# Optimization experiments

Measured on AMD Instinct MI355X. Metric: run time of the kernel, lower is better.

Reference implementation:

```python
import jax, jax.numpy as jnp
import numpy as np

HID, H, HKV, D, INT, S, T = 2048, 16, 8, 128, 6144, 4096, 512
POS = 0          # absolute position of the first token in this prefill chunk
EPS = 1e-6
SCALE = 1.0 / D ** 0.5
REP = H // HKV


def setup_inputs() -> dict:
    key = jax.random.key(0)
    ks = jax.random.split(key, 12)
    w = lambda k, sh: jax.random.normal(k, sh, dtype=jnp.float32) * 0.02

    hidden_conv = jax.random.normal(ks[0], (1, HID, 1, T), dtype=jnp.float32)

    # RoPE tables for absolute positions POS..POS+T-1, HF half-rotation layout
    inv_freq = 1.0 / (10000.0 ** (jnp.arange(0, D, 2, dtype=jnp.float32) / D))
    pos = (POS + jnp.arange(T, dtype=jnp.float32))
    ang = pos[:, None] * inv_freq[None, :]                      # (T, D/2)
    emb = jnp.concatenate([ang, ang], axis=-1)                  # (T, D)
    cos = jnp.cos(emb)[None]                                    # (1, T, D)
    sin = jnp.sin(emb)[None]

    # one-hot write mask: column t has a 1 at row POS+t
    update_mask = jnp.zeros((S, T), jnp.float32).at[POS + jnp.arange(T), jnp.arange(T)].set(1.0)[None, None]
    # causal mask over the cache: slot s visible to token t iff s <= POS+t
    attn_mask = jnp.where(jnp.arange(S)[None, :] <= (POS + jnp.arange(T))[:, None], 0.0, -1e4).astype(jnp.float32)[None, None]

    k_cache = jnp.zeros((1, HKV, S, D), jnp.float32)
    v_cache = jnp.zeros((1, HKV, S, D), jnp.float32)

    return dict(
        hidden_conv=hidden_conv, cos=cos, sin=sin,
        update_mask=update_mask, attn_mask=attn_mask,
        k_cache=k_cache, v_cache=v_cache,
        wq=w(ks[1], (H * D, HID)), wk=w(ks[2], (HKV * D, HID)),
        wv=w(ks[3], (HKV * D, HID)), wo=w(ks[4], (HID, H * D)),
        ln1_w=jnp.ones((HID,), jnp.float32), ln2_w=jnp.ones((HID,), jnp.float32),
        qn_w=jnp.ones((D,), jnp.float32), kn_w=jnp.ones((D,), jnp.float32),
        w_gate_up=w(ks[5], (2 * INT, HID)), w_down=w(ks[6], (HID, INT)),
    )


def _rms(x, w):
    return x * jax.lax.rsqrt(jnp.mean(x * x, axis=-1, keepdims=True) + EPS) * w


def _rotate_half(x):
    x1, x2 = jnp.split(x, 2, axis=-1)
    return jnp.concatenate([-x2, x1], axis=-1)


def reference(hidden_conv, cos, sin, update_mask, attn_mask, k_cache, v_cache,
              wq, wk, wv, wo, ln1_w, ln2_w, qn_w, kn_w, w_gate_up, w_down):
    # (1, HID, 1, T) conv layout -> (1, T, HID)
    x = jnp.transpose(hidden_conv[:, :, 0, :], (0, 2, 1))

    h = _rms(x, ln1_w)
    # 1x1 conv == linear; channel order h*D+d matches view(1,H,D,T)
    q = jnp.einsum('btc,oc->bto', h, wq).reshape(1, T, H, D).transpose(0, 2, 1, 3)    # (1,H,T,D)
    k = jnp.einsum('btc,oc->bto', h, wk).reshape(1, T, HKV, D).transpose(0, 2, 1, 3)  # (1,HKV,T,D)
    v = jnp.einsum('btc,oc->bto', h, wv).reshape(1, T, HKV, D).transpose(0, 2, 1, 3)

    q = _rms(q, qn_w)
    k = _rms(k, kn_w)

    cos_b = cos[:, None]  # (1,1,T,D)
    sin_b = sin[:, None]
    q = q * cos_b + _rotate_half(q) * sin_b
    k = k * cos_b + _rotate_half(k) * sin_b

    # matmul-based KV cache write via one-hot mask (faithful to original)
    k_inc = jnp.matmul(update_mask, k)                 # (1,HKV,S,D)
    v_inc = jnp.matmul(update_mask, v)
    write_any = jnp.sum(update_mask, axis=-1, keepdims=True)  # (1,1,S,1)
    k_full = k_cache * (1.0 - write_any) + k_inc
    v_full = v_cache * (1.0 - write_any) + v_inc

    k_rep = jnp.repeat(k_full, REP, axis=1)            # (1,H,S,D)
    v_rep = jnp.repeat(v_full, REP, axis=1)

    scores = jnp.einsum('bhtd,bhsd->bhts', q, k_rep) * SCALE + attn_mask  # (1,H,T,S)
    attn = jax.nn.softmax(scores, axis=-1)
    out = jnp.einsum('bhts,bhsd->bhtd', attn, v_rep)   # (1,H,T,D)

    o_in = out.transpose(0, 2, 1, 3).reshape(1, T, H * D)
    attn_out = jnp.einsum('btc,oc->bto', o_in, wo)
    hidden = x + attn_out

    h2 = _rms(hidden, ln2_w)
    gate_up = jnp.einsum('btc,oc->bto', h2, w_gate_up)
    gate, up = jnp.split(gate_up, 2, axis=-1)
    mlp = jnp.einsum('bti,oi->bto', jax.nn.silu(gate) * up, w_down)
    hidden = hidden + mlp

    hidden_out = jnp.transpose(hidden, (0, 2, 1))[:, :, None, :]  # back to (1,HID,1,T)
    return hidden_out, k_full, v_full


if __name__ == '__main__':
    outs = reference(**setup_inputs())
    print([o.shape for o in outs])
```

## Files before the change

### kernel.cpp

```cpp
#include <hip/hip_runtime.h>

#define TT 512
#define HIDD 2048
#define NH 16
#define NKV 8
#define DD 128
#define INTR 6144
#define SEQ 4096
#define SCALE 0.08838834764831845f

typedef __attribute__((ext_vector_type(8))) short short8;
typedef __attribute__((ext_vector_type(4))) float floatx4;

static __device__ __forceinline__ unsigned short f2b(float f) {
  unsigned int u = __float_as_uint(f);
  u += 0x7fffu + ((u >> 16) & 1u);
  return (unsigned short)(u >> 16);
}


template <bool H>
struct TileRegs {
  float4 f[4];
  short8 h[2];
};

template <bool H>
static __device__ __forceinline__ void tile_load(const void* __restrict__ src, int ld, int k0,
                                                 int tid, TileRegs<H>& r) {
  if constexpr (H) {
    const unsigned short* s = (const unsigned short*)src;
    const int r0 = tid >> 2, c8 = (tid & 3) << 3;
#pragma unroll
    for (int i = 0; i < 2; ++i)
      r.h[i] = *reinterpret_cast<const short8*>(s + (size_t)(r0 + (i << 6)) * ld + k0 + c8);
  } else {
    const float* s = (const float*)src;
    const int r0 = tid >> 3, c4 = (tid & 7) << 2;
#pragma unroll
    for (int i = 0; i < 4; ++i)
      r.f[i] = *reinterpret_cast<const float4*>(s + (size_t)(r0 + (i << 5)) * ld + k0 + c4);
  }
}

template <bool H>
static __device__ __forceinline__ void tile_store(const TileRegs<H>& r, unsigned short* dst, int tid) {
  if constexpr (H) {
    const int r0 = tid >> 2, c8 = (tid & 3) << 3;
#pragma unroll
    for (int i = 0; i < 2; ++i)
      *reinterpret_cast<short8*>(dst + (r0 + (i << 6)) * 40 + c8) = r.h[i];
  } else {
    const int r0 = tid >> 3, c4 = (tid & 7) << 2;
#pragma unroll
    for (int i = 0; i < 4; ++i) {
      ushort4 o;
      o.x = f2b(r.f[i].x); o.y = f2b(r.f[i].y); o.z = f2b(r.f[i].z); o.w = f2b(r.f[i].w);
      *reinterpret_cast<ushort4*>(dst + (r0 + (i << 5)) * 40 + c4) = o;
    }
  }
}

template <bool A16, bool B16>
static __device__ __forceinline__ void gemm_core(const void* __restrict__ A, int lda,
                                                 const void* __restrict__ B, int ldb,
                                                 int kbeg, int kend, floatx4 acc[4][4],
                                                 unsigned short* As, unsigned short* Bs) {
  const int tid = threadIdx.x;
  const int lane = tid & 63;
  const int wave = tid >> 6;
  const int wr = (wave >> 1) << 6;
  const int wc = (wave & 1) << 6;
  const int lrow = lane & 15;
  const int koff = (lane >> 4) << 3;
  TileRegs<A16> ra;
  TileRegs<B16> rb;
  tile_load<A16>(A, lda, kbeg, tid, ra);
  tile_load<B16>(B, ldb, kbeg, tid, rb);
  for (int k0 = kbeg; k0 < kend; k0 += 32) {
    tile_store<A16>(ra, As, tid);
    tile_store<B16>(rb, Bs, tid);
    __syncthreads();
    if (k0 + 32 < kend) {
      tile_load<A16>(A, lda, k0 + 32, tid, ra);
      tile_load<B16>(B, ldb, k0 + 32, tid, rb);
    }
    short8 af[4], bfr[4];
#pragma unroll
    for (int mi = 0; mi < 4; ++mi)
      af[mi] = *reinterpret_cast<const short8*>(As + (wr + mi * 16 + lrow) * 40 + koff);
#pragma unroll
    for (int ni = 0; ni < 4; ++ni)
      bfr[ni] = *reinterpret_cast<const short8*>(Bs + (wc + ni * 16 + lrow) * 40 + koff);
#pragma unroll
    for (int mi = 0; mi < 4; ++mi)
#pragma unroll
      for (int ni = 0; ni < 4; ++ni)
        acc[mi][ni] = __builtin_amdgcn_mfma_f32_16x16x32_bf16(af[mi], bfr[ni], acc[mi][ni], 0, 0, 0);
    __syncthreads();
  }
}

#define EPI_VARS \
  const int lane = threadIdx.x & 63; \
  const int wave = threadIdx.x >> 6; \
  const int wr = (wave >> 1) << 6;   \
  const int wc = (wave & 1) << 6;    \
  const int lrow = lane & 15;        \
  const int quad = lane >> 4;

#define ZERO_ACC \
  floatx4 acc[4][4]; \
  _Pragma("unroll") for (int mi = 0; mi < 4; ++mi) \
  _Pragma("unroll") for (int ni = 0; ni < 4; ++ni) { floatx4 z = {0.f,0.f,0.f,0.f}; acc[mi][ni] = z; }

template <int S>
static __device__ __forceinline__ void swz(int b, int& mt, int& nt, int& s) {
  mt = (b >> 3) & 3;
  const int gid = ((b >> 5) << 3) | (b & 7);
  nt = gid / S;
  s = gid - nt * S;
}


__global__ __launch_bounds__(256) void k_rms1(const float* __restrict__ conv,
                                              const float* __restrict__ w,
                                              float* __restrict__ xb, float* __restrict__ h1) {
  const int t = blockIdx.x;
  const int tid = threadIdx.x;
  float v[8];
  float ss = 0.f;
#pragma unroll
  for (int i = 0; i < 8; ++i) {
    const int c = tid + (i << 8);
    v[i] = conv[(size_t)c * TT + t];
    ss += v[i] * v[i];
  }
  __shared__ float red[4];
  const int lane = tid & 63, wid = tid >> 6;
#pragma unroll
  for (int o = 32; o; o >>= 1) ss += __shfl_xor(ss, o);
  if (!lane) red[wid] = ss;
  __syncthreads();
  const float tot = red[0] + red[1] + red[2] + red[3];
  const float r = rsqrtf(tot * (1.0f / HIDD) + 1e-6f);
#pragma unroll
  for (int i = 0; i < 8; ++i) {
    const int c = tid + (i << 8);
    xb[(size_t)t * HIDD + c] = v[i];
    h1[(size_t)t * HIDD + c] = v[i] * r * w[c];
  }
}

__global__ __launch_bounds__(256) void k_gemm_qkv(const float* __restrict__ h1,
                                                  const float* __restrict__ wq,
                                                  const float* __restrict__ wk,
                                                  const float* __restrict__ wv,
                                                  float* __restrict__ Pq) {
  __shared__ unsigned short As[128 * 40], Bs[128 * 40];
  int mt, nt, s;
  swz<4>(blockIdx.x, mt, nt, s);
  const int m0 = mt << 7, n0 = nt << 7;
  const float* Bp;
  if (n0 < 2048)      Bp = wq + (size_t)n0 * HIDD;
  else if (n0 < 3072) Bp = wk + (size_t)(n0 - 2048) * HIDD;
  else                Bp = wv + (size_t)(n0 - 3072) * HIDD;
  ZERO_ACC
  gemm_core<false, false>(h1 + (size_t)m0 * HIDD, HIDD, Bp, HIDD, s * 512, s * 512 + 512, acc, As, Bs);
  EPI_VARS
  float* out = Pq + (size_t)s * (TT * 4096);
#pragma unroll
  for (int mi = 0; mi < 4; ++mi)
#pragma unroll
    for (int ni = 0; ni < 4; ++ni)
#pragma unroll
      for (int rr = 0; rr < 4; ++rr) {
        const int row = m0 + wr + mi * 16 + quad * 4 + rr;
        const int col = n0 + wc + ni * 16 + lrow;
        out[(size_t)row * 4096 + col] = acc[mi][ni][rr];
      }
}

__global__ __launch_bounds__(128) void k_rope(const float* __restrict__ Pq,
                                              const float* __restrict__ cosb,
                                              const float* __restrict__ sinb,
                                              const float* __restrict__ qnw,
                                              const float* __restrict__ knw,
                                              unsigned short* __restrict__ qb,
                                              unsigned short* __restrict__ kb,
                                              unsigned short* __restrict__ vtb,
                                              float* __restrict__ kout,
                                              float* __restrict__ vout) {
  const int u = blockIdx.x;
  const int t = blockIdx.y;
  const int d = threadIdx.x;
  __shared__ float red[2];
  __shared__ float sh[DD];
  int slot;
  if (u < NH)            slot = u * DD + d;
  else if (u < NH + NKV) slot = 2048 + (u - NH) * DD + d;
  else                   slot = 3072 + (u - NH - NKV) * DD + d;
  const size_t idx = (size_t)t * 4096 + slot;
  float val = Pq[idx] + Pq[idx + TT * 4096] + Pq[idx + 2 * TT * 4096] + Pq[idx + 3 * TT * 4096];
  if (u < NH + NKV) {
    float ss = val * val;
    const int lane = d & 63, wid = d >> 6;
#pragma unroll
    for (int o = 32; o; o >>= 1) ss += __shfl_xor(ss, o);
    if (!lane) red[wid] = ss;
    __syncthreads();
    const float r = rsqrtf((red[0] + red[1]) * (1.0f / DD) + 1e-6f);
    const float w = (u < NH) ? qnw[d] : knw[d];
    const float nv = val * r * w;
    sh[d] = nv;
    __syncthreads();
    const float partner = sh[d ^ 64];
    const float rh = (d < 64) ? -partner : partner;
    const float o = nv * cosb[(size_t)t * DD + d] + rh * sinb[(size_t)t * DD + d];
    if (u < NH) {
      qb[(size_t)u * TT * DD + (size_t)t * DD + d] = f2b(o);
    } else {
      const int kh = u - NH;
      kout[(size_t)kh * SEQ * DD + (size_t)t * DD + d] = o;
      kb[(size_t)kh * TT * DD + (size_t)t * DD + d] = f2b(o);
    }
  } else {
    const int vh = u - NH - NKV;
    vout[(size_t)vh * SEQ * DD + (size_t)t * DD + d] = val;
    vtb[(size_t)vh * DD * TT + (size_t)d * TT + t] = f2b(val);
  }
}

__global__ __launch_bounds__(256) void k_tail(const float* __restrict__ kc,
                                              const float* __restrict__ vc,
                                              float* __restrict__ ko,
                                              float* __restrict__ vo) {
  const int i = blockIdx.x * 256 + threadIdx.x;
  const int e = i << 2;
  const int s = (e >> 7) & (SEQ - 1);
  if (s >= TT) {
    reinterpret_cast<float4*>(ko)[i] = reinterpret_cast<const float4*>(kc)[i];
    reinterpret_cast<float4*>(vo)[i] = reinterpret_cast<const float4*>(vc)[i];
  }
}

__global__ __launch_bounds__(256) void k_scores(const unsigned short* __restrict__ qb,
                                                const unsigned short* __restrict__ kb,
                                                float* __restrict__ sc) {
  __shared__ unsigned short As[128 * 40], Bs[128 * 40];
  const int m0 = blockIdx.x << 7, n0 = blockIdx.y << 7, h = blockIdx.z;
  ZERO_ACC
  gemm_core<true, true>(qb + (size_t)h * TT * DD + (size_t)m0 * DD, DD,
                        kb + (size_t)(h >> 1) * TT * DD + (size_t)n0 * DD, DD, 0, DD, acc, As, Bs);
  EPI_VARS
  float* out = sc + (size_t)h * TT * TT;
#pragma unroll
  for (int mi = 0; mi < 4; ++mi)
#pragma unroll
    for (int ni = 0; ni < 4; ++ni)
#pragma unroll
      for (int rr = 0; rr < 4; ++rr) {
        const int t = m0 + wr + mi * 16 + quad * 4 + rr;
        const int s = n0 + wc + ni * 16 + lrow;
        float v = acc[mi][ni][rr] * SCALE;
        if (s > t) v += -10000.0f;
        out[(size_t)t * TT + s] = v;
      }
}

__global__ __launch_bounds__(256) void k_softmax(const float* __restrict__ sc,
                                                 unsigned short* __restrict__ Pb) {
  const int h = blockIdx.x >> 9, t = blockIdx.x & 511;
  const int tid = threadIdx.x;
  const float* row = sc + ((size_t)h * TT + t) * TT;
  float v0 = row[tid], v1 = row[tid + 256];
  __shared__ float red[4];
  const int lane = tid & 63, wid = tid >> 6;
  float m = fmaxf(v0, v1);
#pragma unroll
  for (int o = 32; o; o >>= 1) m = fmaxf(m, __shfl_xor(m, o));
  if (!lane) red[wid] = m;
  __syncthreads();
  m = fmaxf(fmaxf(red[0], red[1]), fmaxf(red[2], red[3]));
  const float e0 = __expf(v0 - m), e1 = __expf(v1 - m);
  float s = e0 + e1;
  __syncthreads();
#pragma unroll
  for (int o = 32; o; o >>= 1) s += __shfl_xor(s, o);
  if (!lane) red[wid] = s;
  __syncthreads();
  const float inv = 1.0f / (red[0] + red[1] + red[2] + red[3]);
  unsigned short* orow = Pb + ((size_t)h * TT + t) * TT;
  orow[tid] = f2b(e0 * inv);
  orow[tid + 256] = f2b(e1 * inv);
}

__global__ __launch_bounds__(256) void k_pv(const unsigned short* __restrict__ Pb,
                                            const unsigned short* __restrict__ vtb,
                                            float* __restrict__ Ppv) {
  __shared__ unsigned short As[128 * 40], Bs[128 * 40];
  int mt, h, s;
  swz<4>(blockIdx.x, mt, h, s);
  const int m0 = mt << 7;
  ZERO_ACC
  gemm_core<true, true>(Pb + (size_t)h * TT * TT + (size_t)m0 * TT, TT,
                        vtb + (size_t)(h >> 1) * DD * TT, TT, s * 128, s * 128 + 128, acc, As, Bs);
  EPI_VARS
  float* out = Ppv + (size_t)s * (TT * HIDD);
#pragma unroll
  for (int mi = 0; mi < 4; ++mi)
#pragma unroll
    for (int ni = 0; ni < 4; ++ni)
#pragma unroll
      for (int rr = 0; rr < 4; ++rr) {
        const int row = m0 + wr + mi * 16 + quad * 4 + rr;
        const int col = wc + ni * 16 + lrow;
        out[(size_t)row * HIDD + h * DD + col] = acc[mi][ni][rr];
      }
}

__global__ __launch_bounds__(256) void k_red_pv(const float* __restrict__ Ppv,
                                                float* __restrict__ o_in) {
  const int i = blockIdx.x * 256 + threadIdx.x;
  const float4* p = reinterpret_cast<const float4*>(Ppv);
  float4 a = p[i];
  const float4 b = p[i + 262144], c = p[i + 524288], d = p[i + 786432];
  a.x += b.x + c.x + d.x; a.y += b.y + c.y + d.y;
  a.z += b.z + c.z + d.z; a.w += b.w + c.w + d.w;
  reinterpret_cast<float4*>(o_in)[i] = a;
}

__global__ __launch_bounds__(256) void k_gemm_o(const float* __restrict__ o_in,
                                                const float* __restrict__ wo,
                                                float* __restrict__ Po) {
  __shared__ unsigned short As[128 * 40], Bs[128 * 40];
  int mt, nt, s;
  swz<8>(blockIdx.x, mt, nt, s);
  const int m0 = mt << 7, n0 = nt << 7;
  ZERO_ACC
  gemm_core<false, false>(o_in + (size_t)m0 * HIDD, HIDD, wo + (size_t)n0 * HIDD, HIDD,
                          s * 256, s * 256 + 256, acc, As, Bs);
  EPI_VARS
  float* out = Po + (size_t)s * (TT * HIDD);
#pragma unroll
  for (int mi = 0; mi < 4; ++mi)
#pragma unroll
    for (int ni = 0; ni < 4; ++ni)
#pragma unroll
      for (int rr = 0; rr < 4; ++rr) {
        const int row = m0 + wr + mi * 16 + quad * 4 + rr;
        const int col = n0 + wc + ni * 16 + lrow;
        out[(size_t)row * HIDD + col] = acc[mi][ni][rr];
      }
}

__global__ __launch_bounds__(256) void k_rms2(const float* __restrict__ xb,
                                              const float* __restrict__ Po,
                                              const float* __restrict__ w,
                                              float* __restrict__ hidden,
                                              float* __restrict__ h2) {
  const int t = blockIdx.x;
  const int tid = threadIdx.x;
  float v[8];
  float ss = 0.f;
#pragma unroll
  for (int i = 0; i < 8; ++i) {
    const int c = tid + (i << 8);
    const size_t idx = (size_t)t * HIDD + c;
    float a = xb[idx];
#pragma unroll
    for (int sp = 0; sp < 8; ++sp) a += Po[idx + (size_t)sp * (TT * HIDD)];
    v[i] = a;
    ss += a * a;
  }
  __shared__ float red[4];
  const int lane = tid & 63, wid = tid >> 6;
#pragma unroll
  for (int o = 32; o; o >>= 1) ss += __shfl_xor(ss, o);
  if (!lane) red[wid] = ss;
  __syncthreads();
  const float tot = red[0] + red[1] + red[2] + red[3];
  const float r = rsqrtf(tot * (1.0f / HIDD) + 1e-6f);
#pragma unroll
  for (int i = 0; i < 8; ++i) {
    const int c = tid + (i << 8);
    const size_t idx = (size_t)t * HIDD + c;
    hidden[idx] = v[i];
    h2[idx] = v[i] * r * w[c];
  }
}

__global__ __launch_bounds__(256) void k_gemm_gu(const float* __restrict__ h2,
                                                 const float* __restrict__ wgu,
                                                 float* __restrict__ gu) {
  __shared__ unsigned short As[128 * 40], Bs[128 * 40];
  int mt, nt, s;
  swz<1>(blockIdx.x, mt, nt, s);
  const int m0 = mt << 7, n0 = nt << 7;
  ZERO_ACC
  gemm_core<false, false>(h2 + (size_t)m0 * HIDD, HIDD, wgu + (size_t)n0 * HIDD, HIDD,
                          0, HIDD, acc, As, Bs);
  EPI_VARS
#pragma unroll
  for (int mi = 0; mi < 4; ++mi)
#pragma unroll
    for (int ni = 0; ni < 4; ++ni)
#pragma unroll
      for (int rr = 0; rr < 4; ++rr) {
        const int row = m0 + wr + mi * 16 + quad * 4 + rr;
        const int col = n0 + wc + ni * 16 + lrow;
        gu[(size_t)row * (2 * INTR) + col] = acc[mi][ni][rr];
      }
}

__global__ __launch_bounds__(256) void k_silu(const float* __restrict__ gu,
                                              float* __restrict__ act) {
  const int j = blockIdx.x * 256 + threadIdx.x;
  const int t = blockIdx.y;
  const float g = gu[(size_t)t * (2 * INTR) + j];
  const float u = gu[(size_t)t * (2 * INTR) + INTR + j];
  act[(size_t)t * INTR + j] = g / (1.f + __expf(-g)) * u;
}

__global__ __launch_bounds__(256) void k_gemm_down(const float* __restrict__ act,
                                                   const float* __restrict__ wdn,
                                                   float* __restrict__ Pdn) {
  __shared__ unsigned short As[128 * 40], Bs[128 * 40];
  int mt, nt, s;
  swz<8>(blockIdx.x, mt, nt, s);
  const int m0 = mt << 7, n0 = nt << 7;
  ZERO_ACC
  gemm_core<false, false>(act + (size_t)m0 * INTR, INTR, wdn + (size_t)n0 * INTR, INTR,
                          s * 768, s * 768 + 768, acc, As, Bs);
  EPI_VARS
  float* out = Pdn + (size_t)s * (TT * HIDD);
#pragma unroll
  for (int mi = 0; mi < 4; ++mi)
#pragma unroll
    for (int ni = 0; ni < 4; ++ni)
#pragma unroll
      for (int rr = 0; rr < 4; ++rr) {
        const int row = m0 + wr + mi * 16 + quad * 4 + rr;
        const int col = n0 + wc + ni * 16 + lrow;
        out[(size_t)row * HIDD + col] = acc[mi][ni][rr];
      }
}

__global__ __launch_bounds__(256) void k_final(const float* __restrict__ hidden,
                                               const float* __restrict__ Pdn,
                                               float* __restrict__ out0) {
  __shared__ float tile[32][33];
  const int c0 = blockIdx.x << 5, t0 = blockIdx.y << 5;
  const int tx = threadIdx.x & 31, ty0 = (threadIdx.x >> 5) << 2;
#pragma unroll
  for (int i = 0; i < 4; ++i) {
    const int t = t0 + ty0 + i;
    const size_t idx = (size_t)t * HIDD + c0 + tx;
    float a = hidden[idx];
#pragma unroll
    for (int sp = 0; sp < 8; ++sp) a += Pdn[idx + (size_t)sp * (TT * HIDD)];
    tile[ty0 + i][tx] = a;
  }
  __syncthreads();
#pragma unroll
  for (int i = 0; i < 4; ++i)
    out0[(size_t)(c0 + ty0 + i) * TT + t0 + tx] = tile[tx][ty0 + i];
}

extern "C" void kernel_launch(void* const* d_in, const int* in_sizes, int n_in,
                              void* d_out, int out_size, void* d_ws, size_t ws_size,
                              hipStream_t stream) {
  const float* conv   = (const float*)d_in[0];
  const float* cosb   = (const float*)d_in[1];
  const float* sinb   = (const float*)d_in[2];
  const float* kcache = (const float*)d_in[5];
  const float* vcache = (const float*)d_in[6];
  const float* wq  = (const float*)d_in[7];
  const float* wk  = (const float*)d_in[8];
  const float* wv  = (const float*)d_in[9];
  const float* wo  = (const float*)d_in[10];
  const float* ln1 = (const float*)d_in[11];
  const float* ln2 = (const float*)d_in[12];
  const float* qnw = (const float*)d_in[13];
  const float* knw = (const float*)d_in[14];
  const float* wgu = (const float*)d_in[15];
  const float* wdn = (const float*)d_in[16];

  float* ws = (float*)d_ws;
  float* xb     = ws + 0;
  float* h1     = ws + 1048576;
  float* o_in   = h1;
  float* h2     = ws + 2097152;
  float* hidden = ws + 3145728;
  unsigned short* qb  = (unsigned short*)(ws + 4194304);
  unsigned short* kb  = qb + 1048576;
  unsigned short* vtb = kb + 524288;
  float* act = ws + 5242880;
  float* R   = ws + 8388608;
  float* Pq  = R;
  unsigned short* Pb = (unsigned short*)R;
  float* sc  = R + 2097152;
  float* Ppv = R + 2097152;
  float* Po  = R;
  float* gu  = R;
  float* Pdn = R;

  float* out0 = (float*)d_out;
  float* kout = out0 + 1048576;
  float* vout = kout + 4194304;

  k_rms1<<<TT, 256, 0, stream>>>(conv, ln1, xb, h1);
  k_gemm_qkv<<<512, 256, 0, stream>>>(h1, wq, wk, wv, Pq);
  k_rope<<<dim3(NH + 2 * NKV, TT), 128, 0, stream>>>(Pq, cosb, sinb, qnw, knw, qb, kb, vtb, kout, vout);
  k_tail<<<4096, 256, 0, stream>>>(kcache, vcache, kout, vout);
  k_scores<<<dim3(4, 4, NH), 256, 0, stream>>>(qb, kb, sc);
  k_softmax<<<NH * TT, 256, 0, stream>>>(sc, Pb);
  k_pv<<<256, 256, 0, stream>>>(Pb, vtb, Ppv);
  k_red_pv<<<1024, 256, 0, stream>>>(Ppv, o_in);
  k_gemm_o<<<512, 256, 0, stream>>>(o_in, wo, Po);
  k_rms2<<<TT, 256, 0, stream>>>(xb, Po, ln2, hidden, h2);
  k_gemm_gu<<<384, 256, 0, stream>>>(h2, wgu, gu);
  k_silu<<<dim3(INTR / 256, TT), 256, 0, stream>>>(gu, act);
  k_gemm_down<<<512, 256, 0, stream>>>(act, wdn, Pdn);
  k_final<<<dim3(HIDD / 32, TT / 32), 256, 0, stream>>>(hidden, Pdn, out0);
}
```

Baseline: 501.8 us.

## Double-buffer GEMM LDS, store activations as bf16, shrink M tiles for small GEMMs

```diff
diff --git a/kernel.cpp b/kernel.cpp
--- a/kernel.cpp
+++ b/kernel.cpp
@@ -1,4 +1,5 @@
 #include <hip/hip_runtime.h>
+#include <hip/hip_bf16.h>
 
 #define TT 512
 #define HIDD 2048
@@ -18,101 +19,121 @@
   return (unsigned short)(u >> 16);
 }
 
-
-template <bool H>
-struct TileRegs {
-  float4 f[4];
-  short8 h[2];
-};
-
-template <bool H>
+static __device__ __forceinline__ unsigned int f2b2(float a, float b) {
+  __hip_bfloat162 h = __float22bfloat162_rn(make_float2(a, b));
+  return *reinterpret_cast<unsigned int*>(&h);
+}
+
+
+template <int BM, bool H> struct TR;
+template <> struct TR<128, true>  { short8 v[2]; };
+template <> struct TR<128, false> { float4 v[4]; };
+template <> struct TR<64, true>   { short8 v[1]; };
+template <> struct TR<64, false>  { float4 v[2]; };
+
+template <int BM, bool H>
 static __device__ __forceinline__ void tile_load(const void* __restrict__ src, int ld, int k0,
-                                                 int tid, TileRegs<H>& r) {
+                                                 int tid, TR<BM, H>& r) {
   if constexpr (H) {
     const unsigned short* s = (const unsigned short*)src;
     const int r0 = tid >> 2, c8 = (tid & 3) << 3;
 #pragma unroll
-    for (int i = 0; i < 2; ++i)
-      r.h[i] = *reinterpret_cast<const short8*>(s + (size_t)(r0 + (i << 6)) * ld + k0 + c8);
+    for (int i = 0; i < BM / 64; ++i)
+      r.v[i] = *reinterpret_cast<const short8*>(s + (size_t)(r0 + (i << 6)) * ld + k0 + c8);
   } else {
     const float* s = (const float*)src;
     const int r0 = tid >> 3, c4 = (tid & 7) << 2;
 #pragma unroll
-    for (int i = 0; i < 4; ++i)
-      r.f[i] = *reinterpret_cast<const float4*>(s + (size_t)(r0 + (i << 5)) * ld + k0 + c4);
-  }
-}
-
-template <bool H>
-static __device__ __forceinline__ void tile_store(const TileRegs<H>& r, unsigned short* dst, int tid) {
+    for (int i = 0; i < BM / 32; ++i)
+      r.v[i] = *reinterpret_cast<const float4*>(s + (size_t)(r0 + (i << 5)) * ld + k0 + c4);
+  }
+}
+
+template <int BM, bool H>
+static __device__ __forceinline__ void tile_store(const TR<BM, H>& r, unsigned short* dst, int tid) {
   if constexpr (H) {
     const int r0 = tid >> 2, c8 = (tid & 3) << 3;
 #pragma unroll
-    for (int i = 0; i < 2; ++i)
-      *reinterpret_cast<short8*>(dst + (r0 + (i << 6)) * 40 + c8) = r.h[i];
+    for (int i = 0; i < BM / 64; ++i)
+      *reinterpret_cast<short8*>(dst + (r0 + (i << 6)) * 40 + c8) = r.v[i];
   } else {
     const int r0 = tid >> 3, c4 = (tid & 7) << 2;
 #pragma unroll
-    for (int i = 0; i < 4; ++i) {
-      ushort4 o;
-      o.x = f2b(r.f[i].x); o.y = f2b(r.f[i].y); o.z = f2b(r.f[i].z); o.w = f2b(r.f[i].w);
-      *reinterpret_cast<ushort4*>(dst + (r0 + (i << 5)) * 40 + c4) = o;
+    for (int i = 0; i < BM / 32; ++i) {
+      uint2 o;
+      o.x = f2b2(r.v[i].x, r.v[i].y);
+      o.y = f2b2(r.v[i].z, r.v[i].w);
+      *reinterpret_cast<uint2*>(dst + (r0 + (i << 5)) * 40 + c4) = o;
     }
   }
 }
 
-template <bool A16, bool B16>
+template <int BM, bool A16, bool B16>
 static __device__ __forceinline__ void gemm_core(const void* __restrict__ A, int lda,
                                                  const void* __restrict__ B, int ldb,
-                                                 int kbeg, int kend, floatx4 acc[4][4],
+                                                 int kbeg, int kend, floatx4 (&acc)[BM / 32][4],
                                                  unsigned short* As, unsigned short* Bs) {
+  constexpr int MI = BM / 32;
   const int tid = threadIdx.x;
   const int lane = tid & 63;
   const int wave = tid >> 6;
-  const int wr = (wave >> 1) << 6;
+  const int wr = (wave >> 1) * (BM >> 1);
   const int wc = (wave & 1) << 6;
   const int lrow = lane & 15;
   const int koff = (lane >> 4) << 3;
-  TileRegs<A16> ra;
-  TileRegs<B16> rb;
-  tile_load<A16>(A, lda, kbeg, tid, ra);
-  tile_load<B16>(B, ldb, kbeg, tid, rb);
+  TR<BM, A16> ra;
+  TR<128, B16> rb;
+  tile_load<BM, A16>(A, lda, kbeg, tid, ra);
+  tile_load<128, B16>(B, ldb, kbeg, tid, rb);
+  tile_store<BM, A16>(ra, As, tid);
+  tile_store<128, B16>(rb, Bs, tid);
+  if (kbeg + 32 < kend) {
+    tile_load<BM, A16>(A, lda, kbeg + 32, tid, ra);
+    tile_load<128, B16>(B, ldb, kbeg + 32, tid, rb);
+  }
+  __syncthreads();
+  int p = 0;
   for (int k0 = kbeg; k0 < kend; k0 += 32) {
-    tile_store<A16>(ra, As, tid);
-    tile_store<B16>(rb, Bs, tid);
-    __syncthreads();
+    const unsigned short* Ac = As + p * (BM * 40);
+    const unsigned short* Bc = Bs + p * (128 * 40);
+    unsigned short* An = As + (p ^ 1) * (BM * 40);
+    unsigned short* Bn = Bs + (p ^ 1) * (128 * 40);
+    short8 af[MI], bfr[4];
+#pragma unroll
+    for (int mi = 0; mi < MI; ++mi)
+      af[mi] = *reinterpret_cast<const short8*>(Ac + (wr + mi * 16 + lrow) * 40 + koff);
+#pragma unroll
+    for (int ni = 0; ni < 4; ++ni)
+      bfr[ni] = *reinterpret_cast<const short8*>(Bc + (wc + ni * 16 + lrow) * 40 + koff);
     if (k0 + 32 < kend) {
-      tile_load<A16>(A, lda, k0 + 32, tid, ra);
-      tile_load<B16>(B, ldb, k0 + 32, tid, rb);
+      tile_store<BM, A16>(ra, An, tid);
+      tile_store<128, B16>(rb, Bn, tid);
+      if (k0 + 64 < kend) {
+        tile_load<BM, A16>(A, lda, k0 + 64, tid, ra);
+        tile_load<128, B16>(B, ldb, k0 + 64, tid, rb);
+      }
     }
-    short8 af[4], bfr[4];
-#pragma unroll
-    for (int mi = 0; mi < 4; ++mi)
-      af[mi] = *reinterpret_cast<const short8*>(As + (wr + mi * 16 + lrow) * 40 + koff);
-#pragma unroll
-    for (int ni = 0; ni < 4; ++ni)
-      bfr[ni] = *reinterpret_cast<const short8*>(Bs + (wc + ni * 16 + lrow) * 40 + koff);
-#pragma unroll
-    for (int mi = 0; mi < 4; ++mi)
+#pragma unroll
+    for (int mi = 0; mi < MI; ++mi)
 #pragma unroll
       for (int ni = 0; ni < 4; ++ni)
         acc[mi][ni] = __builtin_amdgcn_mfma_f32_16x16x32_bf16(af[mi], bfr[ni], acc[mi][ni], 0, 0, 0);
     __syncthreads();
+    p ^= 1;
   }
 }
 
 #define EPI_VARS \
   const int lane = threadIdx.x & 63; \
   const int wave = threadIdx.x >> 6; \
-  const int wr = (wave >> 1) << 6;   \
   const int wc = (wave & 1) << 6;    \
   const int lrow = lane & 15;        \
   const int quad = lane >> 4;
 
-#define ZERO_ACC \
-  floatx4 acc[4][4]; \
-  _Pragma("unroll") for (int mi = 0; mi < 4; ++mi) \
-  _Pragma("unroll") for (int ni = 0; ni < 4; ++ni) { floatx4 z = {0.f,0.f,0.f,0.f}; acc[mi][ni] = z; }
+#define ZERO_ACC(MI_) \
+  floatx4 acc[MI_][4]; \
+  _Pragma("unroll") for (int mi = 0; mi < MI_; ++mi) \
+  _Pragma("unroll") for (int ni = 0; ni < 4; ++ni) { floatx4 z = {0.f, 0.f, 0.f, 0.f}; acc[mi][ni] = z; }
 
 template <int S>
 static __device__ __forceinline__ void swz(int b, int& mt, int& nt, int& s) {
@@ -123,41 +144,48 @@
 }
 
 
-__global__ __launch_bounds__(256) void k_rms1(const float* __restrict__ conv,
-                                              const float* __restrict__ w,
-                                              float* __restrict__ xb, float* __restrict__ h1) {
-  const int t = blockIdx.x;
+__global__ __launch_bounds__(1024) void k_rms1(const float* __restrict__ conv,
+                                               const float* __restrict__ w,
+                                               float* __restrict__ xb,
+                                               unsigned short* __restrict__ h1b) {
+  const int t0 = blockIdx.x << 5;
   const int tid = threadIdx.x;
-  float v[8];
+  const int j = tid & 31;
+  const int g = tid >> 5;
+  __shared__ float part[32][32];
+  __shared__ float tile[32][33];
+  __shared__ float rs[32];
   float ss = 0.f;
-#pragma unroll
-  for (int i = 0; i < 8; ++i) {
-    const int c = tid + (i << 8);
-    v[i] = conv[(size_t)c * TT + t];
-    ss += v[i] * v[i];
-  }
-  __shared__ float red[4];
-  const int lane = tid & 63, wid = tid >> 6;
-#pragma unroll
-  for (int o = 32; o; o >>= 1) ss += __shfl_xor(ss, o);
-  if (!lane) red[wid] = ss;
-  __syncthreads();
-  const float tot = red[0] + red[1] + red[2] + red[3];
-  const float r = rsqrtf(tot * (1.0f / HIDD) + 1e-6f);
-#pragma unroll
-  for (int i = 0; i < 8; ++i) {
-    const int c = tid + (i << 8);
-    xb[(size_t)t * HIDD + c] = v[i];
-    h1[(size_t)t * HIDD + c] = v[i] * r * w[c];
-  }
-}
-
-__global__ __launch_bounds__(256) void k_gemm_qkv(const float* __restrict__ h1,
+  for (int c0 = 0; c0 < HIDD; c0 += 32) {
+    const float v = conv[(size_t)(c0 + g) * TT + t0 + j];
+    ss += v * v;
+  }
+  part[g][j] = ss;
+  __syncthreads();
+  if (g == 0) {
+    float tot = 0.f;
+#pragma unroll
+    for (int q = 0; q < 32; ++q) tot += part[q][j];
+    rs[j] = rsqrtf(tot * (1.0f / HIDD) + 1e-6f);
+  }
+  __syncthreads();
+  for (int c0 = 0; c0 < HIDD; c0 += 32) {
+    tile[g][j] = conv[(size_t)(c0 + g) * TT + t0 + j];
+    __syncthreads();
+    const float v = tile[j][g];
+    const float rv = rs[g];
+    xb[(size_t)(t0 + g) * HIDD + c0 + j] = v;
+    h1b[(size_t)(t0 + g) * HIDD + c0 + j] = f2b(v * rv * w[c0 + j]);
+    __syncthreads();
+  }
+}
+
+__global__ __launch_bounds__(256) void k_gemm_qkv(const unsigned short* __restrict__ h1b,
                                                   const float* __restrict__ wq,
                                                   const float* __restrict__ wk,
                                                   const float* __restrict__ wv,
                                                   float* __restrict__ Pq) {
-  __shared__ unsigned short As[128 * 40], Bs[128 * 40];
+  __shared__ unsigned short As[2 * 128 * 40], Bs[2 * 128 * 40];
   int mt, nt, s;
   swz<4>(blockIdx.x, mt, nt, s);
   const int m0 = mt << 7, n0 = nt << 7;
@@ -165,9 +193,10 @@
   if (n0 < 2048)      Bp = wq + (size_t)n0 * HIDD;
   else if (n0 < 3072) Bp = wk + (size_t)(n0 - 2048) * HIDD;
   else                Bp = wv + (size_t)(n0 - 3072) * HIDD;
-  ZERO_ACC
-  gemm_core<false, false>(h1 + (size_t)m0 * HIDD, HIDD, Bp, HIDD, s * 512, s * 512 + 512, acc, As, Bs);
+  ZERO_ACC(4)
+  gemm_core<128, true, false>(h1b + (size_t)m0 * HIDD, HIDD, Bp, HIDD, s * 512, s * 512 + 512, acc, As, Bs);
   EPI_VARS
+  const int wr = (wave >> 1) << 6;
   float* out = Pq + (size_t)s * (TT * 4096);
 #pragma unroll
   for (int mi = 0; mi < 4; ++mi)
@@ -247,15 +276,16 @@
 __global__ __launch_bounds__(256) void k_scores(const unsigned short* __restrict__ qb,
                                                 const unsigned short* __restrict__ kb,
                                                 float* __restrict__ sc) {
-  __shared__ unsigned short As[128 * 40], Bs[128 * 40];
-  const int m0 = blockIdx.x << 7, n0 = blockIdx.y << 7, h = blockIdx.z;
-  ZERO_ACC
-  gemm_core<true, true>(qb + (size_t)h * TT * DD + (size_t)m0 * DD, DD,
-                        kb + (size_t)(h >> 1) * TT * DD + (size_t)n0 * DD, DD, 0, DD, acc, As, Bs);
+  __shared__ unsigned short As[2 * 64 * 40], Bs[2 * 128 * 40];
+  const int m0 = blockIdx.x << 6, n0 = blockIdx.y << 7, h = blockIdx.z;
+  ZERO_ACC(2)
+  gemm_core<64, true, true>(qb + (size_t)h * TT * DD + (size_t)m0 * DD, DD,
+                            kb + (size_t)(h >> 1) * TT * DD + (size_t)n0 * DD, DD, 0, DD, acc, As, Bs);
   EPI_VARS
+  const int wr = (wave >> 1) << 5;
   float* out = sc + (size_t)h * TT * TT;
 #pragma unroll
-  for (int mi = 0; mi < 4; ++mi)
+  for (int mi = 0; mi < 2; ++mi)
 #pragma unroll
     for (int ni = 0; ni < 4; ++ni)
 #pragma unroll
@@ -298,17 +328,16 @@
 __global__ __launch_bounds__(256) void k_pv(const unsigned short* __restrict__ Pb,
                                             const unsigned short* __restrict__ vtb,
                                             float* __restrict__ Ppv) {
-  __shared__ unsigned short As[128 * 40], Bs[128 * 40];
-  int mt, h, s;
-  swz<4>(blockIdx.x, mt, h, s);
-  const int m0 = mt << 7;
-  ZERO_ACC
-  gemm_core<true, true>(Pb + (size_t)h * TT * TT + (size_t)m0 * TT, TT,
-                        vtb + (size_t)(h >> 1) * DD * TT, TT, s * 128, s * 128 + 128, acc, As, Bs);
+  __shared__ unsigned short As[2 * 64 * 40], Bs[2 * 128 * 40];
+  const int m0 = blockIdx.x << 6, h = blockIdx.y, s = blockIdx.z;
+  ZERO_ACC(2)
+  gemm_core<64, true, true>(Pb + (size_t)h * TT * TT + (size_t)m0 * TT, TT,
+                            vtb + (size_t)(h >> 1) * DD * TT, TT, s * 128, s * 128 + 128, acc, As, Bs);
   EPI_VARS
+  const int wr = (wave >> 1) << 5;
   float* out = Ppv + (size_t)s * (TT * HIDD);
 #pragma unroll
-  for (int mi = 0; mi < 4; ++mi)
+  for (int mi = 0; mi < 2; ++mi)
 #pragma unroll
     for (int ni = 0; ni < 4; ++ni)
 #pragma unroll
@@ -320,27 +349,31 @@
 }
 
 __global__ __launch_bounds__(256) void k_red_pv(const float* __restrict__ Ppv,
-                                                float* __restrict__ o_in) {
+                                                unsigned short* __restrict__ o_inb) {
   const int i = blockIdx.x * 256 + threadIdx.x;
   const float4* p = reinterpret_cast<const float4*>(Ppv);
   float4 a = p[i];
   const float4 b = p[i + 262144], c = p[i + 524288], d = p[i + 786432];
   a.x += b.x + c.x + d.x; a.y += b.y + c.y + d.y;
   a.z += b.z + c.z + d.z; a.w += b.w + c.w + d.w;
-  reinterpret_cast<float4*>(o_in)[i] = a;
-}
-
-__global__ __launch_bounds__(256) void k_gemm_o(const float* __restrict__ o_in,
+  uint2 o;
+  o.x = f2b2(a.x, a.y);
+  o.y = f2b2(a.z, a.w);
+  *reinterpret_cast<uint2*>(o_inb + (size_t)i * 4) = o;
+}
+
+__global__ __launch_bounds__(256) void k_gemm_o(const unsigned short* __restrict__ o_inb,
                                                 const float* __restrict__ wo,
                                                 float* __restrict__ Po) {
-  __shared__ unsigned short As[128 * 40], Bs[128 * 40];
+  __shared__ unsigned short As[2 * 128 * 40], Bs[2 * 128 * 40];
   int mt, nt, s;
   swz<8>(blockIdx.x, mt, nt, s);
   const int m0 = mt << 7, n0 = nt << 7;
-  ZERO_ACC
-  gemm_core<false, false>(o_in + (size_t)m0 * HIDD, HIDD, wo + (size_t)n0 * HIDD, HIDD,
-                          s * 256, s * 256 + 256, acc, As, Bs);
+  ZERO_ACC(4)
+  gemm_core<128, true, false>(o_inb + (size_t)m0 * HIDD, HIDD, wo + (size_t)n0 * HIDD, HIDD,
+                              s * 256, s * 256 + 256, acc, As, Bs);
   EPI_VARS
+  const int wr = (wave >> 1) << 6;
   float* out = Po + (size_t)s * (TT * HIDD);
 #pragma unroll
   for (int mi = 0; mi < 4; ++mi)
@@ -358,20 +391,23 @@
                                               const float* __restrict__ Po,
                                               const float* __restrict__ w,
                                               float* __restrict__ hidden,
-                                              float* __restrict__ h2) {
+                                              unsigned short* __restrict__ h2b) {
   const int t = blockIdx.x;
   const int tid = threadIdx.x;
-  float v[8];
+  float2 v[4];
   float ss = 0.f;
 #pragma unroll
-  for (int i = 0; i < 8; ++i) {
-    const int c = tid + (i << 8);
+  for (int i = 0; i < 4; ++i) {
+    const int c = (tid << 1) + (i << 9);
     const size_t idx = (size_t)t * HIDD + c;
-    float a = xb[idx];
-#pragma unroll
-    for (int sp = 0; sp < 8; ++sp) a += Po[idx + (size_t)sp * (TT * HIDD)];
+    float2 a = *reinterpret_cast<const float2*>(xb + idx);
+#pragma unroll
+    for (int sp = 0; sp < 8; ++sp) {
+      const float2 b = *reinterpret_cast<const float2*>(Po + idx + (size_t)sp * (TT * HIDD));
+      a.x += b.x; a.y += b.y;
+    }
     v[i] = a;
-    ss += a * a;
+    ss += a.x * a.x + a.y * a.y;
   }
   __shared__ float red[4];
   const int lane = tid & 63, wid = tid >> 6;
@@ -382,27 +418,29 @@
   const float tot = red[0] + red[1] + red[2] + red[3];
   const float r = rsqrtf(tot * (1.0f / HIDD) + 1e-6f);
 #pragma unroll
-  for (int i = 0; i < 8; ++i) {
-    const int c = tid + (i << 8);
+  for (int i = 0; i < 4; ++i) {
+    const int c = (tid << 1) + (i << 9);
     const size_t idx = (size_t)t * HIDD + c;
-    hidden[idx] = v[i];
-    h2[idx] = v[i] * r * w[c];
-  }
-}
-
-__global__ __launch_bounds__(256) void k_gemm_gu(const float* __restrict__ h2,
+    *reinterpret_cast<float2*>(hidden + idx) = v[i];
+    const float2 wv2 = *reinterpret_cast<const float2*>(w + c);
+    *reinterpret_cast<unsigned int*>(h2b + idx) = f2b2(v[i].x * r * wv2.x, v[i].y * r * wv2.y);
+  }
+}
+
+__global__ __launch_bounds__(256) void k_gemm_gu(const unsigned short* __restrict__ h2b,
                                                  const float* __restrict__ wgu,
                                                  float* __restrict__ gu) {
-  __shared__ unsigned short As[128 * 40], Bs[128 * 40];
-  int mt, nt, s;
-  swz<1>(blockIdx.x, mt, nt, s);
-  const int m0 = mt << 7, n0 = nt << 7;
-  ZERO_ACC
-  gemm_core<false, false>(h2 + (size_t)m0 * HIDD, HIDD, wgu + (size_t)n0 * HIDD, HIDD,
-                          0, HIDD, acc, As, Bs);
+  __shared__ unsigned short As[2 * 64 * 40], Bs[2 * 128 * 40];
+  const int bid = blockIdx.x;
+  const int mt = bid / 96, nt = bid - mt * 96;
+  const int m0 = mt << 6, n0 = nt << 7;
+  ZERO_ACC(2)
+  gemm_core<64, true, false>(h2b + (size_t)m0 * HIDD, HIDD, wgu + (size_t)n0 * HIDD, HIDD,
+                             0, HIDD, acc, As, Bs);
   EPI_VARS
-#pragma unroll
-  for (int mi = 0; mi < 4; ++mi)
+  const int wr = (wave >> 1) << 5;
+#pragma unroll
+  for (int mi = 0; mi < 2; ++mi)
 #pragma unroll
     for (int ni = 0; ni < 4; ++ni)
 #pragma unroll
@@ -414,25 +452,28 @@
 }
 
 __global__ __launch_bounds__(256) void k_silu(const float* __restrict__ gu,
-                                              float* __restrict__ act) {
-  const int j = blockIdx.x * 256 + threadIdx.x;
+                                              unsigned short* __restrict__ actb) {
+  const int j0 = (blockIdx.x * 256 + threadIdx.x) << 1;
   const int t = blockIdx.y;
-  const float g = gu[(size_t)t * (2 * INTR) + j];
-  const float u = gu[(size_t)t * (2 * INTR) + INTR + j];
-  act[(size_t)t * INTR + j] = g / (1.f + __expf(-g)) * u;
-}
-
-__global__ __launch_bounds__(256) void k_gemm_down(const float* __restrict__ act,
+  const float2 g = *reinterpret_cast<const float2*>(gu + (size_t)t * (2 * INTR) + j0);
+  const float2 u = *reinterpret_cast<const float2*>(gu + (size_t)t * (2 * INTR) + INTR + j0);
+  const float a0 = g.x / (1.f + __expf(-g.x)) * u.x;
+  const float a1 = g.y / (1.f + __expf(-g.y)) * u.y;
+  *reinterpret_cast<unsigned int*>(actb + (size_t)t * INTR + j0) = f2b2(a0, a1);
+}
+
+__global__ __launch_bounds__(256) void k_gemm_down(const unsigned short* __restrict__ actb,
                                                    const float* __restrict__ wdn,
                                                    float* __restrict__ Pdn) {
-  __shared__ unsigned short As[128 * 40], Bs[128 * 40];
+  __shared__ unsigned short As[2 * 128 * 40], Bs[2 * 128 * 40];
   int mt, nt, s;
   swz<8>(blockIdx.x, mt, nt, s);
   const int m0 = mt << 7, n0 = nt << 7;
-  ZERO_ACC
-  gemm_core<false, false>(act + (size_t)m0 * INTR, INTR, wdn + (size_t)n0 * INTR, INTR,
-                          s * 768, s * 768 + 768, acc, As, Bs);
+  ZERO_ACC(4)
+  gemm_core<128, true, false>(actb + (size_t)m0 * INTR, INTR, wdn + (size_t)n0 * INTR, INTR,
+                              s * 768, s * 768 + 768, acc, As, Bs);
   EPI_VARS
+  const int wr = (wave >> 1) << 6;
   float* out = Pdn + (size_t)s * (TT * HIDD);
 #pragma unroll
   for (int mi = 0; mi < 4; ++mi)
@@ -487,16 +528,16 @@
   const float* wdn = (const float*)d_in[16];
 
   float* ws = (float*)d_ws;
-  float* xb     = ws + 0;
-  float* h1     = ws + 1048576;
-  float* o_in   = h1;
-  float* h2     = ws + 2097152;
-  float* hidden = ws + 3145728;
-  unsigned short* qb  = (unsigned short*)(ws + 4194304);
+  float* xb = ws + 0;
+  unsigned short* h1b  = (unsigned short*)(ws + 1048576);
+  unsigned short* o_inb = h1b;
+  unsigned short* h2b  = (unsigned short*)(ws + 1572864);
+  float* hidden = ws + 2097152;
+  unsigned short* qb  = (unsigned short*)(ws + 3145728);
   unsigned short* kb  = qb + 1048576;
   unsigned short* vtb = kb + 524288;
-  float* act = ws + 5242880;
-  float* R   = ws + 8388608;
+  unsigned short* actb = (unsigned short*)(ws + 4194304);
+  float* R   = ws + 5767168;
   float* Pq  = R;
   unsigned short* Pb = (unsigned short*)R;
   float* sc  = R + 2097152;
@@ -509,18 +550,18 @@
   float* kout = out0 + 1048576;
   float* vout = kout + 4194304;
 
-  k_rms1<<<TT, 256, 0, stream>>>(conv, ln1, xb, h1);
-  k_gemm_qkv<<<512, 256, 0, stream>>>(h1, wq, wk, wv, Pq);
+  k_rms1<<<16, 1024, 0, stream>>>(conv, ln1, xb, h1b);
+  k_gemm_qkv<<<512, 256, 0, stream>>>(h1b, wq, wk, wv, Pq);
   k_rope<<<dim3(NH + 2 * NKV, TT), 128, 0, stream>>>(Pq, cosb, sinb, qnw, knw, qb, kb, vtb, kout, vout);
   k_tail<<<4096, 256, 0, stream>>>(kcache, vcache, kout, vout);
-  k_scores<<<dim3(4, 4, NH), 256, 0, stream>>>(qb, kb, sc);
+  k_scores<<<dim3(8, 4, NH), 256, 0, stream>>>(qb, kb, sc);
   k_softmax<<<NH * TT, 256, 0, stream>>>(sc, Pb);
-  k_pv<<<256, 256, 0, stream>>>(Pb, vtb, Ppv);
-  k_red_pv<<<1024, 256, 0, stream>>>(Ppv, o_in);
-  k_gemm_o<<<512, 256, 0, stream>>>(o_in, wo, Po);
-  k_rms2<<<TT, 256, 0, stream>>>(xb, Po, ln2, hidden, h2);
-  k_gemm_gu<<<384, 256, 0, stream>>>(h2, wgu, gu);
-  k_silu<<<dim3(INTR / 256, TT), 256, 0, stream>>>(gu, act);
-  k_gemm_down<<<512, 256, 0, stream>>>(act, wdn, Pdn);
+  k_pv<<<dim3(8, NH, 4), 256, 0, stream>>>(Pb, vtb, Ppv);
+  k_red_pv<<<1024, 256, 0, stream>>>(Ppv, o_inb);
+  k_gemm_o<<<512, 256, 0, stream>>>(o_inb, wo, Po);
+  k_rms2<<<TT, 256, 0, stream>>>(xb, Po, ln2, hidden, h2b);
+  k_gemm_gu<<<768, 256, 0, stream>>>(h2b, wgu, gu);
+  k_silu<<<dim3(12, TT), 256, 0, stream>>>(gu, actb);
+  k_gemm_down<<<512, 256, 0, stream>>>(actb, wdn, Pdn);
   k_final<<<dim3(HIDD / 32, TT / 32), 256, 0, stream>>>(hidden, Pdn, out0);
 }
```

Result: faster. 482.4 us (-3.9%).
